# Performance work log

Measured on AMD Instinct MI355X. Metric: run time of the kernel, lower is better.

## Reference

```python
import jax, jax.numpy as jnp
import numpy as np

B, L, D, H = 2, 2048, 512, 8
DK = D // H


def setup_inputs() -> dict:
    key = jax.random.key(0)
    ks = jax.random.split(key, 10)
    s = 1.0 / np.sqrt(D)  # keep pre-softmax logits O(1)
    E = jax.random.normal(ks[0], (B, L, D), jnp.float32)
    Ev = jax.random.normal(ks[1], (B, L, D), jnp.float32)
    # R exactly as matrixR(L+1, D): sinusoid table transposed -> (D, L)
    inv_freq = 1.0 / (10000.0 ** (jnp.arange(0.0, D, 2.0) / D))
    sin_inp = jnp.arange(L, dtype=jnp.float32)[:, None] * inv_freq[None, :]
    R = jnp.concatenate([jnp.sin(sin_inp), jnp.cos(sin_inp)], axis=-1).T
    Wq = jax.random.normal(ks[2], (D, D), jnp.float32) * s
    Wke = jax.random.normal(ks[3], (D, D), jnp.float32) * s
    Wv = jax.random.normal(ks[4], (D, D), jnp.float32) * s
    Wkr = jax.random.normal(ks[5], (D, D), jnp.float32) * s
    cb = jax.random.normal(ks[6], (D,), jnp.float32) * 0.02
    pb = jax.random.normal(ks[7], (D,), jnp.float32) * 0.02
    Wo_w = jax.random.normal(ks[8], (D, D), jnp.float32) * s
    Wo_b = jnp.zeros((D,), jnp.float32)
    ln_g = jnp.ones((D,), jnp.float32)
    ln_b = jnp.zeros((D,), jnp.float32)
    return {"E": E, "Ev": Ev, "R": R, "Wq": Wq, "Wke": Wke, "Wv": Wv,
            "Wkr": Wkr, "cb": cb, "pb": pb, "Wo_w": Wo_w, "Wo_b": Wo_b,
            "ln_g": ln_g, "ln_b": ln_b}


def _shift(b):
    # Transformer-XL shift trick: pad one zero column, reinterpret rows.
    Bn, Hn, Ln, Mn = b.shape
    z = jnp.zeros((Bn, Hn, Ln, 1), b.dtype)
    bp = jnp.concatenate([z, b], axis=3).reshape(Bn, Hn, Mn + 1, Ln)
    return bp[:, :, 1:, :].reshape(Bn, Hn, Ln, Mn)[:, :, :, :Ln]


def reference(E, Ev, R, Wq, Wke, Wv, Wkr, cb, pb, Wo_w, Wo_b, ln_g, ln_b):
    Bn, Ln, Dn = E.shape
    q = (E @ Wq).reshape(Bn, Ln, H, DK).transpose(0, 2, 1, 3)   # (B,H,L,DK)
    k = (E @ Wke).reshape(Bn, Ln, H, DK).transpose(0, 2, 1, 3)  # (B,H,L,DK)
    v = (Ev @ Wv).reshape(Bn, Ln, H, DK).transpose(0, 2, 1, 3)  # (B,H,L,DK)
    Q = (Wkr @ R).reshape(1, H, DK, Ln)                          # (1,H,DK,L)
    kT = jnp.swapaxes(k, -2, -1)                                 # (B,H,DK,L)
    Bsc = q @ Q                                                  # (B,H,L,L)
    Dsc = jnp.broadcast_to(pb.reshape(1, H, 1, DK) @ Q, (Bn, H, Ln, Ln))
    A = (q @ kT) + _shift(Bsc) + (cb.reshape(1, H, 1, DK) @ kT) + _shift(Dsc)
    p = jax.nn.softmax(A, axis=-1)
    Oh = p @ v                                                   # (B,H,L,DK)
    O = Oh.reshape(Bn, Ln, Dn)  # faithful to torch view (no head transpose back)
    y = Ev + O @ Wo_w.T + Wo_b
    mu = jnp.mean(y, axis=-1, keepdims=True)
    var = jnp.var(y, axis=-1, keepdims=True)
    return (y - mu) / jnp.sqrt(var + 1e-5) * ln_g + ln_b
```

## Files before the change

kernel.cpp:

```cpp
#include <hip/hip_runtime.h>
#include <hip/hip_bf16.h>

#define Lc   2048
#define Dc   512
#define Hc   8
#define DKc  64
#define Bc   2
#define NSPLIT 4
#define BHLc (Bc*Hc*Lc)

typedef __attribute__((ext_vector_type(8))) short bf16x8;
typedef __attribute__((ext_vector_type(4))) float f32x4;
typedef __attribute__((ext_vector_type(4))) int   i32x4;
typedef unsigned short u16;

#define MFMA16(a, b, c) __builtin_amdgcn_mfma_f32_16x16x32_bf16((a), (b), (c), 0, 0, 0)

__device__ __forceinline__ u16 f2bf(float x) {
    union { float f; unsigned u; } v; v.f = x;
    unsigned r = v.u + 0x7FFFu + ((v.u >> 16) & 1u);
    return (u16)(r >> 16);
}

union U16x8 { u16 us[8]; i32x4 v; };

template<int TRANS>
__device__ __forceinline__ void stage_tile(u16* sDst, const float* __restrict__ src,
                                           int r0, int k0, int ld, int t)
{
    if (!TRANS) {
        const int row = t >> 2, q = t & 3;
        const float* s = src + (size_t)(r0 + row) * ld + k0 + q * 16;
        float4 f0 = ((const float4*)s)[0];
        float4 f1 = ((const float4*)s)[1];
        float4 f2 = ((const float4*)s)[2];
        float4 f3 = ((const float4*)s)[3];
        U16x8 a, b;
        a.us[0]=f2bf(f0.x); a.us[1]=f2bf(f0.y); a.us[2]=f2bf(f0.z); a.us[3]=f2bf(f0.w);
        a.us[4]=f2bf(f1.x); a.us[5]=f2bf(f1.y); a.us[6]=f2bf(f1.z); a.us[7]=f2bf(f1.w);
        b.us[0]=f2bf(f2.x); b.us[1]=f2bf(f2.y); b.us[2]=f2bf(f2.z); b.us[3]=f2bf(f2.w);
        b.us[4]=f2bf(f3.x); b.us[5]=f2bf(f3.y); b.us[6]=f2bf(f3.z); b.us[7]=f2bf(f3.w);
        const int r7 = row & 7, base = row * 64;
        *(i32x4*)&sDst[base + (((q*2)     ^ r7) << 3)] = a.v;
        *(i32x4*)&sDst[base + (((q*2 + 1) ^ r7) << 3)] = b.v;
    } else {
        const int qq = t & 31, mg = t >> 5;
        const float* s0 = src + (size_t)(k0 + 2*qq) * ld + r0 + mg*8;
        const float* s1 = s0 + ld;
        float4 x0 = ((const float4*)s0)[0], x1 = ((const float4*)s0)[1];
        float4 y0 = ((const float4*)s1)[0], y1 = ((const float4*)s1)[1];
        float e0[8] = {x0.x,x0.y,x0.z,x0.w,x1.x,x1.y,x1.z,x1.w};
        float e1[8] = {y0.x,y0.y,y0.z,y0.w,y1.x,y1.y,y1.z,y1.w};
        unsigned* d32 = (unsigned*)sDst;
        const int g = qq >> 2, off = qq & 3;
#pragma unroll
        for (int e = 0; e < 8; ++e) {
            const int m = mg*8 + e;
            unsigned pk = (unsigned)f2bf(e0[e]) | ((unsigned)f2bf(e1[e]) << 16);
            d32[m*32 + ((g ^ (m & 7)) << 2) + off] = pk;
        }
    }
}

template<int AT, int WT, int OUTMODE, int DUAL, int HASBIAS, int ADDSRC>
__global__ __launch_bounds__(256)
void gemm_mfma(const float* __restrict__ A, const float* __restrict__ W,
               const float* __restrict__ b1, const float* __restrict__ b2,
               const float* __restrict__ add, void* __restrict__ o1v,
               void* __restrict__ o2v, int ldA)
{
    __shared__ __align__(16) u16 sA[64*64];
    __shared__ __align__(16) u16 sB[64*64];
    const int m0 = blockIdx.x * 64, n0 = blockIdx.y * 64;
    const int t = threadIdx.x, lane = t & 63, w = t >> 6;
    const int l15 = lane & 15, lg = lane >> 4;
    const int wm = w >> 1, wn = w & 1;

    f32x4 acc[2][2] = {};

    for (int k0 = 0; k0 < 512; k0 += 64) {
        __syncthreads();
        stage_tile<AT>(sA, A, m0, k0, AT ? ldA : 512, t);
        stage_tile<WT ? 0 : 1>(sB, W, n0, k0, 512, t);
        __syncthreads();
        const int l7 = l15 & 7;
#pragma unroll
        for (int kh = 0; kh < 2; ++kh) {
            bf16x8 av[2], bv[2];
#pragma unroll
            for (int f = 0; f < 2; ++f) {
                const int ra = wm*32 + f*16 + l15;
                av[f] = *(const bf16x8*)&sA[ra*64 + (((kh*4 + lg) ^ l7) << 3)];
                const int rb = wn*32 + f*16 + l15;
                bv[f] = *(const bf16x8*)&sB[rb*64 + (((kh*4 + lg) ^ l7) << 3)];
            }
#pragma unroll
            for (int fm = 0; fm < 2; ++fm)
#pragma unroll
                for (int fn = 0; fn < 2; ++fn)
                    acc[fm][fn] = MFMA16(av[fm], bv[fn], acc[fm][fn]);
        }
    }

#pragma unroll
    for (int fm = 0; fm < 2; ++fm)
#pragma unroll
    for (int fn = 0; fn < 2; ++fn) {
        const int colg = n0 + wn*32 + fn*16 + l15;
#pragma unroll
        for (int r = 0; r < 4; ++r) {
            const int row = m0 + wm*32 + fm*16 + lg*4 + r;
            float v = acc[fm][fn][r];
            if (OUTMODE == 0) {
                if (HASBIAS) v += b1[colg];
                if (ADDSRC)  v += add[(size_t)row*512 + colg];
                ((float*)o1v)[(size_t)row*512 + colg] = v;
            } else if (OUTMODE == 1) {
                if (HASBIAS) v += b1[colg];
                const int h = colg >> 6, dk = colg & 63;
                const int bb = row >> 11, ii = row & 2047;
                const size_t idx = (((size_t)(bb*Hc + h)*Lc + ii) << 6) + dk;
                ((u16*)o1v)[idx] = f2bf(v);
                if (DUAL)
                    ((u16*)o2v)[idx] = f2bf(acc[fm][fn][r] + b2[colg]);
            } else if (OUTMODE == 2) {
                const int h = row >> 6, dk = row & 63;
                const int bb = colg >> 11, ii = colg & 2047;
                ((u16*)o1v)[((size_t)(bb*Hc + h)*DKc + dk)*Lc + ii] = f2bf(v);
            } else {
                const int h = colg >> 6, dk = colg & 63;
                ((u16*)o1v)[(((size_t)h*Lc + row) << 6) + dk] = f2bf(v);
            }
        }
    }
}

__global__ __launch_bounds__(256)
void attn_mfma(const u16* __restrict__ qc, const u16* __restrict__ qp,
               const u16* __restrict__ kk, const u16* __restrict__ vt,
               const u16* __restrict__ qrt, float* __restrict__ Opart,
               float* __restrict__ mlbuf)
{
    __shared__ __align__(16) u16 sK[64*64];
    __shared__ __align__(16) u16 sV[64*64];
    __shared__ __align__(16) u16 sBand[128*64];
    __shared__ __align__(16) float sP2[4*1344];

    const int orig = ((blockIdx.x & 7) << 8) | (blockIdx.x >> 3);
    const int it = orig & 31;
    const int sp = (orig >> 5) & (NSPLIT - 1);
    const int bh = orig >> 7;
    const int h = bh & 7, b = bh >> 3;
    const int i0 = it << 6;
    const int t = threadIdx.x;
    const int lane = t & 63, w = t >> 6;
    const int l15 = lane & 15, lg = lane >> 4;

    float* p2w = sP2 + w * 1344;
    u16*   spw = (u16*)p2w;

    const size_t ho = (size_t)(b*Hc + h) * (Lc * DKc);
    const u16* qcH  = qc  + ho;
    const u16* qpH  = qp  + ho;
    const u16* kH   = kk  + ho;
    const u16* vtH  = vt  + ho;
    const u16* qrtH = qrt + (size_t)h * (Lc * DKc);

    const int rowA = i0 + w*16 + l15;
    const int rowB = (rowA + 1 < Lc) ? rowA + 1 : Lc - 1;
    bf16x8 qc0 = *(const bf16x8*)(qcH + (size_t)rowA*64 +      lg*8);
    bf16x8 qc1 = *(const bf16x8*)(qcH + (size_t)rowA*64 + 32 + lg*8);
    bf16x8 qa0 = *(const bf16x8*)(qpH + (size_t)rowA*64 +      lg*8);
    bf16x8 qa1 = *(const bf16x8*)(qpH + (size_t)rowA*64 + 32 + lg*8);
    bf16x8 qb0 = *(const bf16x8*)(qpH + (size_t)rowB*64 +      lg*8);
    bf16x8 qb1 = *(const bf16x8*)(qpH + (size_t)rowB*64 + 32 + lg*8);

    f32x4 oacc[4] = {};
    float mrow[4] = {-1e30f, -1e30f, -1e30f, -1e30f};
    float lsum[4] = {0.f, 0.f, 0.f, 0.f};

    for (int jq = 0; jq < 32/NSPLIT; ++jq) {
        const int jt = sp * (32/NSPLIT) + jq;
        const int j0 = jt << 6;
        const int dBase = j0 - i0 - 63;
        __syncthreads();
#pragma unroll
        for (int p = 0; p < 2; ++p) {
            const int s = t + p*256, row = s >> 3, g = s & 7;
            const int sl = row*64 + ((g ^ (row & 7)) << 3);
            *(i32x4*)&sK[sl] = *(const i32x4*)(kH  + (size_t)(j0+row)*64 + g*8);
            *(i32x4*)&sV[sl] = *(const i32x4*)(vtH + (size_t)row*Lc + j0 + g*8);
        }
#pragma unroll
        for (int p = 0; p < 4; ++p) {
            const int s = t + p*256, dd = s >> 3, g = s & 7;
            const int d = dBase + dd;
            const int m = (d <= 0) ? (d + Lc - 1) : ((d >= 2) ? (d - 2) : 0);
            *(i32x4*)&sBand[dd*64 + ((g ^ (dd & 7)) << 3)] =
                *(const i32x4*)(qrtH + (size_t)m*64 + g*8);
        }
        __syncthreads();

        __builtin_amdgcn_s_setprio(1);
        f32x4 sc[4];
#pragma unroll
        for (int nb = 0; nb < 4; ++nb) {
            const int row = nb*16 + l15;
            bf16x8 k0 = *(const bf16x8*)&sK[row*64 + ((( lg    ) ^ (row & 7)) << 3)];
            bf16x8 k1 = *(const bf16x8*)&sK[row*64 + (((lg + 4) ^ (row & 7)) << 3)];
            f32x4 z = {0.f, 0.f, 0.f, 0.f};
            z = MFMA16(qc0, k0, z);
            z = MFMA16(qc1, k1, z);
            sc[nb] = z;
        }

#pragma unroll
        for (int cbl = 0; cbl < 5; ++cbl) {
            const int cb  = cbl + 3 - w;
            const int row = cb*16 + l15;
            bf16x8 b0 = *(const bf16x8*)&sBand[row*64 + ((( lg    ) ^ (row & 7)) << 3)];
            bf16x8 b1 = *(const bf16x8*)&sBand[row*64 + (((lg + 4) ^ (row & 7)) << 3)];
            f32x4 z = {0.f, 0.f, 0.f, 0.f};
            if ((dBase + cb*16) >= 1) {
                z = MFMA16(qb0, b0, z);
                z = MFMA16(qb1, b1, z);
            } else {
                z = MFMA16(qa0, b0, z);
                z = MFMA16(qa1, b1, z);
            }
            if (!(cbl == 4 && l15 == 15)) {
                const int base = (cbl*16 + l15)*17 + lg*4;
                p2w[base+0] = z[0]; p2w[base+1] = z[1];
                p2w[base+2] = z[2]; p2w[base+3] = z[3];
            }
        }
        __builtin_amdgcn_s_setprio(0);
        __asm__ volatile("" ::: "memory");

        float pm[4];
#pragma unroll
        for (int r = 0; r < 4; ++r) {
            const int blm = lg*4 + r;
            const int blg = w*16 + blm;
#pragma unroll
            for (int nb = 0; nb < 4; ++nb) {
                const int jl = nb*16 + l15;
                const int d  = dBase + jl - blg + 63;
                const float pv = p2w[(jl - blm + 15)*17 + blm];
                sc[nb][r] += (d == 1) ? 0.f : pv;
            }
            pm[r] = fmaxf(fmaxf(sc[0][r], sc[1][r]), fmaxf(sc[2][r], sc[3][r]));
        }

        const float over = fmaxf(fmaxf(pm[0]-mrow[0], pm[1]-mrow[1]),
                                 fmaxf(pm[2]-mrow[2], pm[3]-mrow[3]));
        if (__all(over <= 8.0f)) {
#pragma unroll
            for (int r = 0; r < 4; ++r) {
                float p0 = __expf(sc[0][r] - mrow[r]);
                float p1 = __expf(sc[1][r] - mrow[r]);
                float p2 = __expf(sc[2][r] - mrow[r]);
                float p3 = __expf(sc[3][r] - mrow[r]);
                sc[0][r] = p0; sc[1][r] = p1; sc[2][r] = p2; sc[3][r] = p3;
                lsum[r] += p0 + p1 + p2 + p3;
            }
        } else {
            float fsc[4];
#pragma unroll
            for (int r = 0; r < 4; ++r) {
                float mx = pm[r];
                mx = fmaxf(mx, __shfl_xor(mx, 1, 64));
                mx = fmaxf(mx, __shfl_xor(mx, 2, 64));
                mx = fmaxf(mx, __shfl_xor(mx, 4, 64));
                mx = fmaxf(mx, __shfl_xor(mx, 8, 64));
                const float mnew = fmaxf(mrow[r], mx);
                const float fac  = __expf(mrow[r] - mnew);
                mrow[r] = mnew;
                float p0 = __expf(sc[0][r] - mnew);
                float p1 = __expf(sc[1][r] - mnew);
                float p2 = __expf(sc[2][r] - mnew);
                float p3 = __expf(sc[3][r] - mnew);
                sc[0][r] = p0; sc[1][r] = p1; sc[2][r] = p2; sc[3][r] = p3;
                lsum[r] = lsum[r] * fac + (p0 + p1 + p2 + p3);
                fsc[r] = fac;
            }
#pragma unroll
            for (int nb = 0; nb < 4; ++nb)
#pragma unroll
                for (int r = 0; r < 4; ++r)
                    oacc[nb][r] *= fsc[r];
        }
        __asm__ volatile("" ::: "memory");

#pragma unroll
        for (int r = 0; r < 4; ++r) {
            const int blm = lg*4 + r;
#pragma unroll
            for (int nb = 0; nb < 4; ++nb) {
                const int jl = nb*16 + l15;
                spw[blm*64 + (((jl >> 3) ^ (blm & 7)) << 3) + (jl & 7)] = f2bf(sc[nb][r]);
            }
        }
        __asm__ volatile("" ::: "memory");

        __builtin_amdgcn_s_setprio(1);
        {
            bf16x8 pa0 = *(const bf16x8*)&spw[l15*64 + ((( lg    ) ^ (l15 & 7)) << 3)];
            bf16x8 pa1 = *(const bf16x8*)&spw[l15*64 + (((lg + 4) ^ (l15 & 7)) << 3)];
#pragma unroll
            for (int nb = 0; nb < 4; ++nb) {
                const int row = nb*16 + l15;
                bf16x8 v0 = *(const bf16x8*)&sV[row*64 + ((( lg    ) ^ (row & 7)) << 3)];
                bf16x8 v1 = *(const bf16x8*)&sV[row*64 + (((lg + 4) ^ (row & 7)) << 3)];
                oacc[nb] = MFMA16(pa0, v0, oacc[nb]);
                oacc[nb] = MFMA16(pa1, v1, oacc[nb]);
            }
        }
        __builtin_amdgcn_s_setprio(0);
    }

    float* Op = Opart + (size_t)sp * (Bc*Hc*Lc*DKc) + ho;
#pragma unroll
    for (int r = 0; r < 4; ++r) {
        float ls = lsum[r];
        ls += __shfl_xor(ls, 1, 64);
        ls += __shfl_xor(ls, 2, 64);
        ls += __shfl_xor(ls, 4, 64);
        ls += __shfl_xor(ls, 8, 64);
        const int bl = w*16 + lg*4 + r;
#pragma unroll
        for (int nb = 0; nb < 4; ++nb)
            Op[(size_t)(i0 + bl)*64 + nb*16 + l15] = oacc[nb][r];
        if (l15 == 0) {
            const int rglob = (b*Hc + h)*Lc + i0 + bl;
            *(float2*)&mlbuf[((size_t)sp*BHLc + rglob)*2] = make_float2(mrow[r], ls);
        }
    }
}

__global__ __launch_bounds__(256)
void attn_combine(const float* __restrict__ Opart, const float* __restrict__ mlbuf,
                  float* __restrict__ Oh)
{
    const int t = threadIdx.x;
    const int row = blockIdx.x * 64 + (t >> 2);
    const int q = t & 3;
    const size_t NQl = (size_t)Bc * Hc * Lc * DKc;

    float m[NSPLIT], l[NSPLIT];
#pragma unroll
    for (int s = 0; s < NSPLIT; ++s) {
        float2 ml = *(const float2*)&mlbuf[((size_t)s*BHLc + row)*2];
        m[s] = ml.x; l[s] = ml.y;
    }
    float M = fmaxf(fmaxf(m[0], m[1]), fmaxf(m[2], m[3]));
    float wgt[NSPLIT], wsum = 0.f;
#pragma unroll
    for (int s = 0; s < NSPLIT; ++s) { wgt[s] = __expf(m[s] - M); wsum += l[s]*wgt[s]; }
    const float inv = 1.f / wsum;

    f32x4 acc[4] = {};
#pragma unroll
    for (int s = 0; s < NSPLIT; ++s) {
        const f32x4* src = (const f32x4*)(Opart + (size_t)s*NQl + (size_t)row*64 + q*16);
#pragma unroll
        for (int u = 0; u < 4; ++u)
            acc[u] += src[u] * wgt[s];
    }
    f32x4* dst = (f32x4*)(Oh + (size_t)row*64 + q*16);
#pragma unroll
    for (int u = 0; u < 4; ++u)
        dst[u] = acc[u] * inv;
}

__global__ __launch_bounds__(256)
void ln_kernel(const float* __restrict__ yr, const float* __restrict__ g,
               const float* __restrict__ be, float* __restrict__ out)
{
    const int row = blockIdx.x;
    const int t   = threadIdx.x;
    const float2 v = *(const float2*)&yr[(size_t)row * 512 + t*2];
    float sum = v.x + v.y;
    float sq  = v.x*v.x + v.y*v.y;
#pragma unroll
    for (int off = 1; off < 64; off <<= 1) {
        sum += __shfl_xor(sum, off, 64);
        sq  += __shfl_xor(sq,  off, 64);
    }
    __shared__ float ssum[4], ssq[4];
    if ((t & 63) == 0) { ssum[t >> 6] = sum; ssq[t >> 6] = sq; }
    __syncthreads();
    sum = ssum[0] + ssum[1] + ssum[2] + ssum[3];
    sq  = ssq[0]  + ssq[1]  + ssq[2]  + ssq[3];
    const float mu   = sum * (1.f / 512.f);
    const float var  = sq * (1.f / 512.f) - mu * mu;
    const float rstd = rsqrtf(var + 1e-5f);
    float2 ov;
    ov.x = (v.x - mu) * rstd * g[t*2+0] + be[t*2+0];
    ov.y = (v.y - mu) * rstd * g[t*2+1] + be[t*2+1];
    *(float2*)&out[(size_t)row * 512 + t*2] = ov;
}

extern "C" void kernel_launch(void* const* d_in, const int* in_sizes, int n_in,
                              void* d_out, int out_size, void* d_ws, size_t ws_size,
                              hipStream_t stream)
{
    const float* E    = (const float*)d_in[0];
    const float* Ev   = (const float*)d_in[1];
    const float* R    = (const float*)d_in[2];
    const float* Wq   = (const float*)d_in[3];
    const float* Wke  = (const float*)d_in[4];
    const float* Wv   = (const float*)d_in[5];
    const float* Wkr  = (const float*)d_in[6];
    const float* cb   = (const float*)d_in[7];
    const float* pb   = (const float*)d_in[8];
    const float* Wo_w = (const float*)d_in[9];
    const float* Wo_b = (const float*)d_in[10];
    const float* ln_g = (const float*)d_in[11];
    const float* ln_b = (const float*)d_in[12];
    float* out = (float*)d_out;

    const size_t NQ = (size_t)Bc * Hc * Lc * DKc;
    const size_t NR = (size_t)Hc * Lc * DKc;
    const size_t need = (4*NQ + NR)*2 + (size_t)NSPLIT*NQ*4 + (size_t)NSPLIT*BHLc*2*4;
    if (ws_size < need) return;

    u16* qcB  = (u16*)d_ws;
    u16* qpB  = qcB + NQ;
    u16* kB   = qpB + NQ;
    u16* vtB  = kB  + NQ;
    u16* qrtB = vtB + NQ;
    float* Opart = (float*)(qrtB + NR);
    float* mlbuf = Opart + (size_t)NSPLIT*NQ;
    float* Oh = Opart;
    float* yr = Opart + NQ;

    dim3 blk(256);
    gemm_mfma<0,0,1,1,1,0><<<dim3(64,8), blk, 0, stream>>>(E, Wq, cb, pb, nullptr, qcB, qpB, 512);
    gemm_mfma<0,0,1,0,0,0><<<dim3(64,8), blk, 0, stream>>>(E, Wke, nullptr, nullptr, nullptr, kB, nullptr, 512);
    gemm_mfma<1,1,2,0,0,0><<<dim3(8,64), blk, 0, stream>>>(Wv, Ev, nullptr, nullptr, nullptr, vtB, nullptr, 512);
    gemm_mfma<1,1,3,0,0,0><<<dim3(32,8), blk, 0, stream>>>(R, Wkr, nullptr, nullptr, nullptr, qrtB, nullptr, 2048);
    attn_mfma<<<dim3(Bc*Hc*NSPLIT*32), blk, 0, stream>>>(qcB, qpB, kB, vtB, qrtB, Opart, mlbuf);
    attn_combine<<<dim3(BHLc/64), blk, 0, stream>>>(Opart, mlbuf, Oh);
    gemm_mfma<0,1,0,0,1,1><<<dim3(64,8), blk, 0, stream>>>(Oh, Wo_w, Wo_b, nullptr, Ev, yr, nullptr, 512);
    ln_kernel<<<dim3(4096), blk, 0, stream>>>(yr, ln_g, ln_b, out);
}
```

Before: 180.2 us.

## Store attention partials in bf16, fuse Q/K projections, hoist V fragment loads

Attention partial outputs and the combined head output are now written and read as bf16 instead of fp32. This halves the memory traffic through attn_combine and the output-projection GEMM, whose A operand is loaded directly as bf16 without conversion. The Q and K projections are merged into one kernel that stages the E tile once and feeds two accumulator sets. V fragments are loaded from LDS earlier in the attention loop so the loads overlap softmax work. In exchange, the unnormalized partial outputs lose precision, and the extra live registers may lower occupancy.

```diff
diff --git a/kernel.cpp b/kernel.cpp
--- a/kernel.cpp
+++ b/kernel.cpp
@@ -20,6 +20,9 @@
     union { float f; unsigned u; } v; v.f = x;
     unsigned r = v.u + 0x7FFFu + ((v.u >> 16) & 1u);
     return (u16)(r >> 16);
+}
+__device__ __forceinline__ float bf2f(u16 x) {
+    union { unsigned u; float f; } v; v.u = ((unsigned)x) << 16; return v.f;
 }
 
 union U16x8 { u16 us[8]; i32x4 v; };
@@ -62,7 +65,7 @@
     }
 }
 
-template<int AT, int WT, int OUTMODE, int DUAL, int HASBIAS, int ADDSRC>
+template<int AT, int WT, int OUTMODE, int DUAL, int HASBIAS, int ADDSRC, int ABF = 0>
 __global__ __launch_bounds__(256)
 void gemm_mfma(const float* __restrict__ A, const float* __restrict__ W,
                const float* __restrict__ b1, const float* __restrict__ b2,
@@ -80,7 +83,18 @@
 
     for (int k0 = 0; k0 < 512; k0 += 64) {
         __syncthreads();
-        stage_tile<AT>(sA, A, m0, k0, AT ? ldA : 512, t);
+        if (ABF) {
+            const u16* A16 = (const u16*)A;
+            const int row = t >> 2, q = t & 3;
+            const u16* s = A16 + (size_t)(m0 + row) * 512 + k0 + q*16;
+            i32x4 v0 = ((const i32x4*)s)[0];
+            i32x4 v1 = ((const i32x4*)s)[1];
+            const int r7 = row & 7, base = row * 64;
+            *(i32x4*)&sA[base + (((q*2)     ^ r7) << 3)] = v0;
+            *(i32x4*)&sA[base + (((q*2 + 1) ^ r7) << 3)] = v1;
+        } else {
+            stage_tile<AT>(sA, A, m0, k0, AT ? ldA : 512, t);
+        }
         stage_tile<WT ? 0 : 1>(sB, W, n0, k0, 512, t);
         __syncthreads();
         const int l7 = l15 & 7;
@@ -136,9 +150,72 @@
 }
 
 __global__ __launch_bounds__(256)
+void gemm_qkp(const float* __restrict__ E, const float* __restrict__ Wq,
+              const float* __restrict__ Wke, const float* __restrict__ cb,
+              const float* __restrict__ pb, u16* __restrict__ qcB,
+              u16* __restrict__ qpB, u16* __restrict__ kB)
+{
+    __shared__ __align__(16) u16 sA[64*64];
+    __shared__ __align__(16) u16 sB1[64*64];
+    __shared__ __align__(16) u16 sB2[64*64];
+    const int m0 = blockIdx.x * 64, n0 = blockIdx.y * 64;
+    const int t = threadIdx.x, lane = t & 63, w = t >> 6;
+    const int l15 = lane & 15, lg = lane >> 4;
+    const int wm = w >> 1, wn = w & 1;
+
+    f32x4 acc1[2][2] = {};
+    f32x4 acc2[2][2] = {};
+
+    for (int k0 = 0; k0 < 512; k0 += 64) {
+        __syncthreads();
+        stage_tile<0>(sA,  E,   m0, k0, 512, t);
+        stage_tile<1>(sB1, Wq,  n0, k0, 512, t);
+        stage_tile<1>(sB2, Wke, n0, k0, 512, t);
+        __syncthreads();
+        const int l7 = l15 & 7;
+#pragma unroll
+        for (int kh = 0; kh < 2; ++kh) {
+            bf16x8 av[2], b1v[2], b2v[2];
+#pragma unroll
+            for (int f = 0; f < 2; ++f) {
+                const int ra = wm*32 + f*16 + l15;
+                av[f]  = *(const bf16x8*)&sA [ra*64 + (((kh*4 + lg) ^ l7) << 3)];
+                const int rb = wn*32 + f*16 + l15;
+                b1v[f] = *(const bf16x8*)&sB1[rb*64 + (((kh*4 + lg) ^ l7) << 3)];
+                b2v[f] = *(const bf16x8*)&sB2[rb*64 + (((kh*4 + lg) ^ l7) << 3)];
+            }
+#pragma unroll
+            for (int fm = 0; fm < 2; ++fm)
+#pragma unroll
+                for (int fn = 0; fn < 2; ++fn) {
+                    acc1[fm][fn] = MFMA16(av[fm], b1v[fn], acc1[fm][fn]);
+                    acc2[fm][fn] = MFMA16(av[fm], b2v[fn], acc2[fm][fn]);
+                }
+        }
+    }
+
+#pragma unroll
+    for (int fm = 0; fm < 2; ++fm)
+#pragma unroll
+    for (int fn = 0; fn < 2; ++fn) {
+        const int colg = n0 + wn*32 + fn*16 + l15;
+        const int h = colg >> 6, dk = colg & 63;
+#pragma unroll
+        for (int r = 0; r < 4; ++r) {
+            const int row = m0 + wm*32 + fm*16 + lg*4 + r;
+            const int bb = row >> 11, ii = row & 2047;
+            const size_t idx = (((size_t)(bb*Hc + h)*Lc + ii) << 6) + dk;
+            qcB[idx] = f2bf(acc1[fm][fn][r] + cb[colg]);
+            qpB[idx] = f2bf(acc1[fm][fn][r] + pb[colg]);
+            kB[idx]  = f2bf(acc2[fm][fn][r]);
+        }
+    }
+}
+
+__global__ __launch_bounds__(256)
 void attn_mfma(const u16* __restrict__ qc, const u16* __restrict__ qp,
                const u16* __restrict__ kk, const u16* __restrict__ vt,
-               const u16* __restrict__ qrt, float* __restrict__ Opart,
+               const u16* __restrict__ qrt, u16* __restrict__ Opart,
                float* __restrict__ mlbuf)
 {
     __shared__ __align__(16) u16 sK[64*64];
@@ -236,6 +313,14 @@
         }
         __builtin_amdgcn_s_setprio(0);
         __asm__ volatile("" ::: "memory");
+
+        bf16x8 vr[4][2];
+#pragma unroll
+        for (int nb = 0; nb < 4; ++nb) {
+            const int row = nb*16 + l15;
+            vr[nb][0] = *(const bf16x8*)&sV[row*64 + ((( lg    ) ^ (row & 7)) << 3)];
+            vr[nb][1] = *(const bf16x8*)&sV[row*64 + (((lg + 4) ^ (row & 7)) << 3)];
+        }
 
         float pm[4];
 #pragma unroll
@@ -309,17 +394,14 @@
             bf16x8 pa1 = *(const bf16x8*)&spw[l15*64 + (((lg + 4) ^ (l15 & 7)) << 3)];
 #pragma unroll
             for (int nb = 0; nb < 4; ++nb) {
-                const int row = nb*16 + l15;
-                bf16x8 v0 = *(const bf16x8*)&sV[row*64 + ((( lg    ) ^ (row & 7)) << 3)];
-                bf16x8 v1 = *(const bf16x8*)&sV[row*64 + (((lg + 4) ^ (row & 7)) << 3)];
-                oacc[nb] = MFMA16(pa0, v0, oacc[nb]);
-                oacc[nb] = MFMA16(pa1, v1, oacc[nb]);
+                oacc[nb] = MFMA16(pa0, vr[nb][0], oacc[nb]);
+                oacc[nb] = MFMA16(pa1, vr[nb][1], oacc[nb]);
             }
         }
         __builtin_amdgcn_s_setprio(0);
     }
 
-    float* Op = Opart + (size_t)sp * (Bc*Hc*Lc*DKc) + ho;
+    u16* Op = Opart + (size_t)sp * (Bc*Hc*Lc*DKc) + ho;
 #pragma unroll
     for (int r = 0; r < 4; ++r) {
         float ls = lsum[r];
@@ -330,7 +412,7 @@
         const int bl = w*16 + lg*4 + r;
 #pragma unroll
         for (int nb = 0; nb < 4; ++nb)
-            Op[(size_t)(i0 + bl)*64 + nb*16 + l15] = oacc[nb][r];
+            Op[(size_t)(i0 + bl)*64 + nb*16 + l15] = f2bf(oacc[nb][r]);
         if (l15 == 0) {
             const int rglob = (b*Hc + h)*Lc + i0 + bl;
             *(float2*)&mlbuf[((size_t)sp*BHLc + rglob)*2] = make_float2(mrow[r], ls);
@@ -339,8 +421,8 @@
 }
 
 __global__ __launch_bounds__(256)
-void attn_combine(const float* __restrict__ Opart, const float* __restrict__ mlbuf,
-                  float* __restrict__ Oh)
+void attn_combine(const u16* __restrict__ Opart, const float* __restrict__ mlbuf,
+                  u16* __restrict__ Oh)
 {
     const int t = threadIdx.x;
     const int row = blockIdx.x * 64 + (t >> 2);
@@ -359,18 +441,25 @@
     for (int s = 0; s < NSPLIT; ++s) { wgt[s] = __expf(m[s] - M); wsum += l[s]*wgt[s]; }
     const float inv = 1.f / wsum;
 
-    f32x4 acc[4] = {};
+    float acc[16] = {};
 #pragma unroll
     for (int s = 0; s < NSPLIT; ++s) {
-        const f32x4* src = (const f32x4*)(Opart + (size_t)s*NQl + (size_t)row*64 + q*16);
-#pragma unroll
-        for (int u = 0; u < 4; ++u)
-            acc[u] += src[u] * wgt[s];
-    }
-    f32x4* dst = (f32x4*)(Oh + (size_t)row*64 + q*16);
-#pragma unroll
-    for (int u = 0; u < 4; ++u)
-        dst[u] = acc[u] * inv;
+        const i32x4* src = (const i32x4*)(Opart + (size_t)s*NQl + (size_t)row*64 + q*16);
+        U16x8 a, b; a.v = src[0]; b.v = src[1];
+#pragma unroll
+        for (int e = 0; e < 8; ++e) {
+            acc[e]   += wgt[s] * bf2f(a.us[e]);
+            acc[8+e] += wgt[s] * bf2f(b.us[e]);
+        }
+    }
+    U16x8 o0, o1;
+#pragma unroll
+    for (int e = 0; e < 8; ++e) {
+        o0.us[e] = f2bf(acc[e]   * inv);
+        o1.us[e] = f2bf(acc[8+e] * inv);
+    }
+    i32x4* dst = (i32x4*)(Oh + (size_t)row*64 + q*16);
+    dst[0] = o0.v; dst[1] = o1.v;
 }
 
 __global__ __launch_bounds__(256)
@@ -422,7 +511,7 @@
 
     const size_t NQ = (size_t)Bc * Hc * Lc * DKc;
     const size_t NR = (size_t)Hc * Lc * DKc;
-    const size_t need = (4*NQ + NR)*2 + (size_t)NSPLIT*NQ*4 + (size_t)NSPLIT*BHLc*2*4;
+    const size_t need = (4*NQ + NR)*2 + (size_t)NSPLIT*NQ*2 + (size_t)NSPLIT*BHLc*2*4;
     if (ws_size < need) return;
 
     u16* qcB  = (u16*)d_ws;
@@ -430,18 +519,17 @@
     u16* kB   = qpB + NQ;
     u16* vtB  = kB  + NQ;
     u16* qrtB = vtB + NQ;
-    float* Opart = (float*)(qrtB + NR);
-    float* mlbuf = Opart + (size_t)NSPLIT*NQ;
-    float* Oh = Opart;
-    float* yr = Opart + NQ;
+    u16* Opart = qrtB + NR;
+    float* mlbuf = (float*)(Opart + (size_t)NSPLIT*NQ);
+    u16* Oh16 = Opart;
+    float* yr = (float*)(Opart + NQ);
 
     dim3 blk(256);
-    gemm_mfma<0,0,1,1,1,0><<<dim3(64,8), blk, 0, stream>>>(E, Wq, cb, pb, nullptr, qcB, qpB, 512);
-    gemm_mfma<0,0,1,0,0,0><<<dim3(64,8), blk, 0, stream>>>(E, Wke, nullptr, nullptr, nullptr, kB, nullptr, 512);
+    gemm_qkp<<<dim3(64,8), blk, 0, stream>>>(E, Wq, Wke, cb, pb, qcB, qpB, kB);
     gemm_mfma<1,1,2,0,0,0><<<dim3(8,64), blk, 0, stream>>>(Wv, Ev, nullptr, nullptr, nullptr, vtB, nullptr, 512);
     gemm_mfma<1,1,3,0,0,0><<<dim3(32,8), blk, 0, stream>>>(R, Wkr, nullptr, nullptr, nullptr, qrtB, nullptr, 2048);
     attn_mfma<<<dim3(Bc*Hc*NSPLIT*32), blk, 0, stream>>>(qcB, qpB, kB, vtB, qrtB, Opart, mlbuf);
-    attn_combine<<<dim3(BHLc/64), blk, 0, stream>>>(Opart, mlbuf, Oh);
-    gemm_mfma<0,1,0,0,1,1><<<dim3(64,8), blk, 0, stream>>>(Oh, Wo_w, Wo_b, nullptr, Ev, yr, nullptr, 512);
+    attn_combine<<<dim3(BHLc/64), blk, 0, stream>>>(Opart, mlbuf, Oh16);
+    gemm_mfma<0,1,0,0,1,1,1><<<dim3(64,8), blk, 0, stream>>>((const float*)Oh16, Wo_w, Wo_b, nullptr, Ev, yr, nullptr, 512);
     ln_kernel<<<dim3(4096), blk, 0, stream>>>(yr, ln_g, ln_b, out);
 }
```

Result: slower. 227.5 us (+26.3%).
